# Kernel optimization log

Measured on AMD Instinct MI355X. Metric: run time of the kernel, lower is better.

Reference implementation:

```python
import jax, jax.numpy as jnp
import numpy as np

LN_EPS = 1e-5

def setup_inputs() -> dict:
    key = jax.random.key(0)
    ks = jax.random.split(key, 8)
    B, L, D = 1, 768, 1024
    DP, H, NB = 128, 128, 64
    s = lambda fan_in: 1.0 / np.sqrt(fan_in)
    return {
        "x": jax.random.normal(ks[0], (B, L, D), dtype=jnp.float32),
        "W_down": jax.random.normal(ks[1], (DP, D), dtype=jnp.float32) * s(D),
        "b_down": jax.random.normal(ks[2], (DP,), dtype=jnp.float32) * s(D),
        "W1": jax.random.normal(ks[3], (H, DP), dtype=jnp.float32) * s(DP),
        "b1": jax.random.normal(ks[4], (H,), dtype=jnp.float32) * s(DP),
        "ln_g": jnp.ones((H,), dtype=jnp.float32),
        "ln_b": jnp.zeros((H,), dtype=jnp.float32),
        "W2": jax.random.normal(ks[5], (NB, H), dtype=jnp.float32) * s(H),
        "b2": jax.random.normal(ks[6], (NB,), dtype=jnp.float32) * s(H),
    }

def reference(x, W_down, b_down, W1, b1, ln_g, ln_b, W2, b2):
    # downproject: [B,L,D] -> [B,L,DP]
    xd = jnp.einsum("bld,pd->blp", x, W_down) + b_down
    q, k = jnp.split(xd, 2, axis=-1)                      # each [B,L,DP/2]
    prod = q[:, None, :, :] * k[:, :, None, :]            # [B,L,L,DP/2]
    diff = q[:, None, :, :] - k[:, :, None, :]            # [B,L,L,DP/2]
    h = jnp.concatenate([prod, diff], axis=-1)            # [B,L,L,DP]
    h = jnp.einsum("bijp,hp->bijh", h, W1) + b1           # [B,L,L,H]
    h = jax.nn.gelu(h, approximate=False)                 # torch GELU is exact erf form
    mu = jnp.mean(h, axis=-1, keepdims=True)
    var = jnp.mean(jnp.square(h - mu), axis=-1, keepdims=True)
    h = (h - mu) * jax.lax.rsqrt(var + LN_EPS) * ln_g + ln_b
    out = jnp.einsum("bijh,nh->bijn", h, W2) + b2         # [B,L,L,NB]
    return out
```

## Files before the change

### kernel.cpp

```cpp
#include <hip/hip_runtime.h>
#include <hip/hip_bf16.h>

#define LL 768
#define DD 1024
#define DP 128
#define HP 64
#define HH 128
#define NB 64

typedef float f32x4 __attribute__((ext_vector_type(4)));
typedef __bf16 bf16x8 __attribute__((ext_vector_type(8)));
typedef __bf16 bf16x4 __attribute__((ext_vector_type(4)));

__device__ __forceinline__ float gelu_exact(float x) {
    const float z = fabsf(x) * 0.70710678118654752f;
    const float t = __builtin_amdgcn_rcpf(__builtin_fmaf(0.3275911f, z, 1.0f));
    float p = __builtin_fmaf(t, 1.061405429f, -1.453152027f);
    p = __builtin_fmaf(t, p, 1.421413741f);
    p = __builtin_fmaf(t, p, -0.284496736f);
    p = __builtin_fmaf(t, p, 0.254829592f);
    p = p * t;
    const float e = __expf(-z * z);
    const float erfz = __builtin_fmaf(-p, e, 1.0f);
    const float phi = 0.5f * (1.0f + copysignf(erfz, x));
    return x * phi;
}

__global__ __launch_bounds__(256) void prep_kernel(
    const float* __restrict__ x, const float* __restrict__ Wd,
    const float* __restrict__ bd, const float* __restrict__ W1,
    const float* __restrict__ b1, const float* __restrict__ W2,
    const float* __restrict__ lng, const float* __restrict__ lnb,
    const float* __restrict__ b2,
    __hip_bfloat16* __restrict__ qb, float* __restrict__ kf,
    float* __restrict__ A2, float* __restrict__ Bv,
    __hip_bfloat16* __restrict__ W2gb, float* __restrict__ c2b)
{
    __shared__ __align__(16) float xs[4 * DD];
    __shared__ __align__(16) float xdl[4 * 128];
    const int bid  = blockIdx.x;
    const int tid  = threadIdx.x;
    const int w    = tid >> 6;
    const int lane = tid & 63;

    if (bid >= 192) {
        const int nb = bid - 192;
        for (int e = tid; e < 8 * HH; e += 256) {
            const int n = nb * 8 + (e >> 7), h = e & 127;
            W2gb[n * HH + h] = __float2bfloat16(W2[n * HH + h] * lng[h]);
        }
        #pragma unroll
        for (int rr = 0; rr < 2; ++rr) {
            const int n = nb * 8 + w * 2 + rr;
            float s = W2[n * HH + lane] * lnb[lane]
                    + W2[n * HH + 64 + lane] * lnb[64 + lane];
            #pragma unroll
            for (int m = 1; m < 64; m <<= 1) s += __shfl_xor(s, m);
            if (lane == 0) c2b[n] = s + b2[n];
        }
        return;
    }

    const int l0 = bid * 4;
    const float4* xg = (const float4*)(x + (size_t)l0 * DD);
    float4* xs4 = (float4*)xs;
    for (int idx = tid; idx < 4 * DD / 4; idx += 256) xs4[idx] = xg[idx];
    __syncthreads();

    const int p = tid & 127;
    const int rg = tid >> 7;
    float acc[2] = {0.f, 0.f};
    #pragma unroll 8
    for (int c = 0; c < DD; c += 4) {
        float4 wv = *(const float4*)(Wd + (size_t)p * DD + c);
        #pragma unroll
        for (int rr = 0; rr < 2; ++rr) {
            float4 xv = *(const float4*)(xs + (rg * 2 + rr) * DD + c);
            acc[rr] += wv.x * xv.x + wv.y * xv.y + wv.z * xv.z + wv.w * xv.w;
        }
    }
    const float bdp = bd[p];
    #pragma unroll
    for (int rr = 0; rr < 2; ++rr) {
        const int row = rg * 2 + rr;
        const float v = acc[rr] + bdp;
        xdl[row * 128 + p] = v;
        if (p < HP) qb[(size_t)(l0 + row) * HP + p] = __float2bfloat16(v);
        else        kf[(size_t)(l0 + row) * HP + (p - HP)] = v;
    }
    __syncthreads();

    const int h = tid & 127;
    const int sel = tid >> 7;
    float a4[4] = {0.f, 0.f, 0.f, 0.f};
    #pragma unroll
    for (int c = 0; c < HP; c += 4) {
        float4 wv = *(const float4*)(W1 + (size_t)h * DP + HP + c);
        #pragma unroll
        for (int r = 0; r < 4; ++r) {
            float4 xv = *(const float4*)(xdl + r * 128 + (sel ? HP : 0) + c);
            a4[r] += wv.x * xv.x + wv.y * xv.y + wv.z * xv.z + wv.w * xv.w;
        }
    }
    if (sel == 0) {
        const float bb = b1[h];
        #pragma unroll
        for (int r = 0; r < 4; ++r)
            A2[(size_t)(l0 + r) * HH + h] = a4[r] + bb;
    } else {
        #pragma unroll
        for (int r = 0; r < 4; ++r)
            Bv[(size_t)(l0 + r) * HH + h] = a4[r];
    }
}

__global__ __launch_bounds__(256, 3) void main_kernel(
    const float* __restrict__ W1, const __hip_bfloat16* __restrict__ W2gb,
    const __hip_bfloat16* __restrict__ qb, const float* __restrict__ kf,
    const float* __restrict__ A2, const float* __restrict__ Bv,
    const float* __restrict__ c2b, float* __restrict__ out)
{
    __shared__ __align__(16) unsigned char smem[49152];
    __bf16* Mi   = (__bf16*)smem;
    __bf16* qt   = (__bf16*)(smem + 16384);
    __bf16* W2gs = (__bf16*)(smem + 32768);
    __bf16* hbuf = (__bf16*)smem;

    const int tid  = threadIdx.x;
    const int lane = tid & 63;
    const int w    = tid >> 6;
    const int lo   = lane & 15;
    const int g4   = lane >> 4;
    const int sw   = (lo & 7) << 3;
    const int i    = blockIdx.y;
    const int j0   = blockIdx.x * 128;

    {
        const int hrow = tid >> 1;
        const int pb = (tid & 1) * 32;
        const int swr = (hrow & 7) << 3;
        const float* w1r = W1 + (size_t)hrow * DP + pb;
        const float* kfr = kf + (size_t)i * HP + pb;
        #pragma unroll
        for (int m = 0; m < 4; ++m) {
            float4 w0 = *(const float4*)(w1r + m * 8);
            float4 w1v = *(const float4*)(w1r + m * 8 + 4);
            float4 k0 = *(const float4*)(kfr + m * 8);
            float4 k1 = *(const float4*)(kfr + m * 8 + 4);
            bf16x8 t;
            t[0] = (__bf16)(w0.x * k0.x); t[1] = (__bf16)(w0.y * k0.y);
            t[2] = (__bf16)(w0.z * k0.z); t[3] = (__bf16)(w0.w * k0.w);
            t[4] = (__bf16)(w1v.x * k1.x); t[5] = (__bf16)(w1v.y * k1.y);
            t[6] = (__bf16)(w1v.z * k1.z); t[7] = (__bf16)(w1v.w * k1.w);
            *(bf16x8*)&Mi[hrow * 64 + ((pb + m * 8) ^ swr)] = t;
        }
    }
    {
        const int jl = tid >> 1;
        const int pb = (tid & 1) * 32;
        const int swr = (jl & 7) << 3;
        const unsigned short* src = (const unsigned short*)qb + (size_t)(j0 + jl) * HP + pb;
        #pragma unroll
        for (int m = 0; m < 4; ++m) {
            uint4 v = *(const uint4*)(src + m * 8);
            *(uint4*)&qt[jl * 64 + ((pb + m * 8) ^ swr)] = v;
        }
    }
    {
        const int n = tid >> 2;
        const int hb0 = (tid & 3) * 32;
        const int swr = (n & 7) << 3;
        const unsigned short* src = (const unsigned short*)W2gb + (size_t)n * HH + hb0;
        #pragma unroll
        for (int m = 0; m < 4; ++m) {
            uint4 v = *(const uint4*)(src + m * 8);
            *(uint4*)&W2gs[n * 128 + ((hb0 + m * 8) ^ swr)] = v;
        }
    }
    __syncthreads();

    f32x4 acc[2][8];
    #pragma unroll
    for (int a = 0; a < 2; ++a)
        #pragma unroll
        for (int b = 0; b < 8; ++b)
            #pragma unroll
            for (int e = 0; e < 4; ++e) acc[a][b][e] = 0.f;

    #pragma unroll
    for (int kk = 0; kk < 2; ++kk) {
        const int colx = (kk * 32 + g4 * 8) ^ sw;
        bf16x8 bq[2];
        #pragma unroll
        for (int jt = 0; jt < 2; ++jt)
            bq[jt] = *(const bf16x8*)&qt[(32 * w + jt * 16 + lo) * 64 + colx];
        #pragma unroll
        for (int ht = 0; ht < 8; ++ht) {
            bf16x8 am = *(const bf16x8*)&Mi[(ht * 16 + lo) * 64 + colx];
            #pragma unroll
            for (int jt = 0; jt < 2; ++jt)
                acc[jt][ht] = __builtin_amdgcn_mfma_f32_16x16x32_bf16(am, bq[jt], acc[jt][ht], 0, 0, 0);
        }
    }

    __syncthreads();

    #pragma unroll
    for (int jt = 0; jt < 2; ++jt) {
        const int jl = 32 * w + jt * 16 + lo;
        const float* a2r = A2 + (size_t)(j0 + jl) * HH;
        const float* bvr = Bv + (size_t)i * HH;
        float s = 0.f, ss = 0.f;
        #pragma unroll
        for (int ht = 0; ht < 8; ++ht) {
            const int h4 = ht * 16 + g4 * 4;
            f32x4 a2v = *(const f32x4*)&a2r[h4];
            f32x4 bvv = *(const f32x4*)&bvr[h4];
            #pragma unroll
            for (int r = 0; r < 4; ++r) {
                float v = acc[jt][ht][r] + a2v[r] - bvv[r];
                float g = gelu_exact(v);
                acc[jt][ht][r] = g;
                s += g;
                ss = __builtin_fmaf(g, g, ss);
            }
        }
        s  += __shfl_xor(s, 16);  s  += __shfl_xor(s, 32);
        ss += __shfl_xor(ss, 16); ss += __shfl_xor(ss, 32);
        const float mu   = s * (1.0f / 128.0f);
        const float var  = ss * (1.0f / 128.0f) - mu * mu;
        const float rstd = rsqrtf(var + 1e-5f);
        const float nmr  = -mu * rstd;
        #pragma unroll
        for (int ht = 0; ht < 8; ++ht) {
            bf16x4 t;
            #pragma unroll
            for (int r = 0; r < 4; ++r)
                t[r] = (__bf16)__builtin_fmaf(acc[jt][ht][r], rstd, nmr);
            *(bf16x4*)&hbuf[jl * 128 + ((ht * 16 + g4 * 4) ^ sw)] = t;
        }
    }
    asm volatile("s_waitcnt lgkmcnt(0)" ::: "memory");
    __builtin_amdgcn_sched_barrier(0);

    f32x4 acc2[2][4];
    #pragma unroll
    for (int a = 0; a < 2; ++a)
        #pragma unroll
        for (int b = 0; b < 4; ++b)
            #pragma unroll
            for (int e = 0; e < 4; ++e) acc2[a][b][e] = 0.f;

    #pragma unroll
    for (int kk = 0; kk < 4; ++kk) {
        const int colx = (kk * 32 + g4 * 8) ^ sw;
        bf16x8 bh[2];
        #pragma unroll
        for (int jt = 0; jt < 2; ++jt)
            bh[jt] = *(const bf16x8*)&hbuf[(32 * w + jt * 16 + lo) * 128 + colx];
        #pragma unroll
        for (int nt2 = 0; nt2 < 4; ++nt2) {
            bf16x8 aw = *(const bf16x8*)&W2gs[(nt2 * 16 + lo) * 128 + colx];
            #pragma unroll
            for (int jt = 0; jt < 2; ++jt)
                acc2[jt][nt2] = __builtin_amdgcn_mfma_f32_16x16x32_bf16(aw, bh[jt], acc2[jt][nt2], 0, 0, 0);
        }
    }

    #pragma unroll
    for (int jt = 0; jt < 2; ++jt) {
        const int j = j0 + 32 * w + jt * 16 + lo;
        const size_t base = ((size_t)i * LL + j) * NB;
        #pragma unroll
        for (int nt2 = 0; nt2 < 4; ++nt2) {
            const int n4 = nt2 * 16 + g4 * 4;
            f32x4 c2bv = *(const f32x4*)&c2b[n4];
            f32x4 o;
            #pragma unroll
            for (int r = 0; r < 4; ++r)
                o[r] = acc2[jt][nt2][r] + c2bv[r];
            *(f32x4*)&out[base + n4] = o;
        }
    }
}

extern "C" void kernel_launch(void* const* d_in, const int* in_sizes, int n_in,
                              void* d_out, int out_size, void* d_ws, size_t ws_size,
                              hipStream_t stream) {
    const float* x   = (const float*)d_in[0];
    const float* Wd  = (const float*)d_in[1];
    const float* bd  = (const float*)d_in[2];
    const float* W1  = (const float*)d_in[3];
    const float* b1  = (const float*)d_in[4];
    const float* lng = (const float*)d_in[5];
    const float* lnb = (const float*)d_in[6];
    const float* W2  = (const float*)d_in[7];
    const float* b2  = (const float*)d_in[8];
    float* out = (float*)d_out;

    char* ws = (char*)d_ws;
    __hip_bfloat16* qb   = (__hip_bfloat16*)ws;
    float* kf    = (float*)(ws + 98304);
    float* A2    = (float*)(ws + 294912);
    float* Bv    = (float*)(ws + 688128);
    __hip_bfloat16* W2gb = (__hip_bfloat16*)(ws + 1081344);
    float* c2b   = (float*)(ws + 1097728);

    prep_kernel<<<200, 256, 0, stream>>>(x, Wd, bd, W1, b1, W2, lng, lnb, b2,
                                         qb, kf, A2, Bv, W2gb, c2b);
    dim3 grid(6, 768);
    main_kernel<<<grid, 256, 0, stream>>>(W1, W2gb, qb, kf, A2, Bv, c2b, out);
}
```

Measured before the change: 135.6 us.

## Alias W2 tile into q region and split second GEMM per half-tile

Shared memory drops from 48KB to 32KB. The W2 tile now reuses the q-tile region once the first GEMM finishes, and the H buffer shrinks to 16 rows per wave. The LayerNorm and second GEMM now run one 16-row half at a time, which also cuts the live acc2 registers in half. The W2 global loads are issued into registers before the first GEMM's results are consumed, so their latency overlaps compute. The cost is an extra barrier and less MFMA reuse of each loaded W2 fragment in the second GEMM.

Result: slower. 155.0 us (+14.3%).

```diff
diff --git a/kernel.cpp b/kernel.cpp
--- a/kernel.cpp
+++ b/kernel.cpp
@@ -120,11 +120,11 @@
     const float* __restrict__ A2, const float* __restrict__ Bv,
     const float* __restrict__ c2b, float* __restrict__ out)
 {
-    __shared__ __align__(16) unsigned char smem[49152];
+    __shared__ __align__(16) unsigned char smem[32768];
     __bf16* Mi   = (__bf16*)smem;
     __bf16* qt   = (__bf16*)(smem + 16384);
-    __bf16* W2gs = (__bf16*)(smem + 32768);
     __bf16* hbuf = (__bf16*)smem;
+    __bf16* W2gs = (__bf16*)(smem + 16384);
 
     const int tid  = threadIdx.x;
     const int lane = tid & 63;
@@ -166,50 +166,57 @@
             *(uint4*)&qt[jl * 64 + ((pb + m * 8) ^ swr)] = v;
         }
     }
+    __syncthreads();
+
+    f32x4 acc[2][8];
+    #pragma unroll
+    for (int a = 0; a < 2; ++a)
+        #pragma unroll
+        for (int b = 0; b < 8; ++b)
+            #pragma unroll
+            for (int e = 0; e < 4; ++e) acc[a][b][e] = 0.f;
+
+    #pragma unroll
+    for (int kk = 0; kk < 2; ++kk) {
+        const int colx = (kk * 32 + g4 * 8) ^ sw;
+        bf16x8 bq[2];
+        #pragma unroll
+        for (int jt = 0; jt < 2; ++jt)
+            bq[jt] = *(const bf16x8*)&qt[(32 * w + jt * 16 + lo) * 64 + colx];
+        #pragma unroll
+        for (int ht = 0; ht < 8; ++ht) {
+            bf16x8 am = *(const bf16x8*)&Mi[(ht * 16 + lo) * 64 + colx];
+            #pragma unroll
+            for (int jt = 0; jt < 2; ++jt)
+                acc[jt][ht] = __builtin_amdgcn_mfma_f32_16x16x32_bf16(am, bq[jt], acc[jt][ht], 0, 0, 0);
+        }
+    }
+
+    uint4 wreg[4];
+    {
+        const int n = tid >> 2;
+        const int hb0 = (tid & 3) * 32;
+        const unsigned short* src = (const unsigned short*)W2gb + (size_t)n * HH + hb0;
+        #pragma unroll
+        for (int m = 0; m < 4; ++m)
+            wreg[m] = *(const uint4*)(src + m * 8);
+    }
+    __syncthreads();
     {
         const int n = tid >> 2;
         const int hb0 = (tid & 3) * 32;
         const int swr = (n & 7) << 3;
-        const unsigned short* src = (const unsigned short*)W2gb + (size_t)n * HH + hb0;
-        #pragma unroll
-        for (int m = 0; m < 4; ++m) {
-            uint4 v = *(const uint4*)(src + m * 8);
-            *(uint4*)&W2gs[n * 128 + ((hb0 + m * 8) ^ swr)] = v;
-        }
-    }
-    __syncthreads();
-
-    f32x4 acc[2][8];
-    #pragma unroll
-    for (int a = 0; a < 2; ++a)
-        #pragma unroll
-        for (int b = 0; b < 8; ++b)
-            #pragma unroll
-            for (int e = 0; e < 4; ++e) acc[a][b][e] = 0.f;
-
-    #pragma unroll
-    for (int kk = 0; kk < 2; ++kk) {
-        const int colx = (kk * 32 + g4 * 8) ^ sw;
-        bf16x8 bq[2];
-        #pragma unroll
-        for (int jt = 0; jt < 2; ++jt)
-            bq[jt] = *(const bf16x8*)&qt[(32 * w + jt * 16 + lo) * 64 + colx];
-        #pragma unroll
-        for (int ht = 0; ht < 8; ++ht) {
-            bf16x8 am = *(const bf16x8*)&Mi[(ht * 16 + lo) * 64 + colx];
-            #pragma unroll
-            for (int jt = 0; jt < 2; ++jt)
-                acc[jt][ht] = __builtin_amdgcn_mfma_f32_16x16x32_bf16(am, bq[jt], acc[jt][ht], 0, 0, 0);
-        }
-    }
-
-    __syncthreads();
+        #pragma unroll
+        for (int m = 0; m < 4; ++m)
+            *(uint4*)&W2gs[n * 128 + ((hb0 + m * 8) ^ swr)] = wreg[m];
+    }
+
+    const float* a2base = A2 + (size_t)(j0 + 32 * w + lo) * HH;
+    const float* bvr    = Bv + (size_t)i * HH;
 
     #pragma unroll
     for (int jt = 0; jt < 2; ++jt) {
-        const int jl = 32 * w + jt * 16 + lo;
-        const float* a2r = A2 + (size_t)(j0 + jl) * HH;
-        const float* bvr = Bv + (size_t)i * HH;
+        const float* a2r = a2base + (size_t)(jt * 16) * HH;
         float s = 0.f, ss = 0.f;
         #pragma unroll
         for (int ht = 0; ht < 8; ++ht) {
@@ -231,44 +238,40 @@
         const float var  = ss * (1.0f / 128.0f) - mu * mu;
         const float rstd = rsqrtf(var + 1e-5f);
         const float nmr  = -mu * rstd;
+        const int hrow = w * 16 + lo;
         #pragma unroll
         for (int ht = 0; ht < 8; ++ht) {
             bf16x4 t;
             #pragma unroll
             for (int r = 0; r < 4; ++r)
                 t[r] = (__bf16)__builtin_fmaf(acc[jt][ht][r], rstd, nmr);
-            *(bf16x4*)&hbuf[jl * 128 + ((ht * 16 + g4 * 4) ^ sw)] = t;
-        }
-    }
-    asm volatile("s_waitcnt lgkmcnt(0)" ::: "memory");
-    __builtin_amdgcn_sched_barrier(0);
-
-    f32x4 acc2[2][4];
-    #pragma unroll
-    for (int a = 0; a < 2; ++a)
+            *(bf16x4*)&hbuf[hrow * 128 + ((ht * 16 + g4 * 4) ^ sw)] = t;
+        }
+
+        if (jt == 0) {
+            __syncthreads();
+        } else {
+            asm volatile("s_waitcnt lgkmcnt(0)" ::: "memory");
+            __builtin_amdgcn_sched_barrier(0);
+        }
+
+        f32x4 acc2[4];
         #pragma unroll
         for (int b = 0; b < 4; ++b)
             #pragma unroll
-            for (int e = 0; e < 4; ++e) acc2[a][b][e] = 0.f;
-
-    #pragma unroll
-    for (int kk = 0; kk < 4; ++kk) {
-        const int colx = (kk * 32 + g4 * 8) ^ sw;
-        bf16x8 bh[2];
-        #pragma unroll
-        for (int jt = 0; jt < 2; ++jt)
-            bh[jt] = *(const bf16x8*)&hbuf[(32 * w + jt * 16 + lo) * 128 + colx];
-        #pragma unroll
-        for (int nt2 = 0; nt2 < 4; ++nt2) {
-            bf16x8 aw = *(const bf16x8*)&W2gs[(nt2 * 16 + lo) * 128 + colx];
-            #pragma unroll
-            for (int jt = 0; jt < 2; ++jt)
-                acc2[jt][nt2] = __builtin_amdgcn_mfma_f32_16x16x32_bf16(aw, bh[jt], acc2[jt][nt2], 0, 0, 0);
-        }
-    }
-
-    #pragma unroll
-    for (int jt = 0; jt < 2; ++jt) {
+            for (int e = 0; e < 4; ++e) acc2[b][e] = 0.f;
+
+        #pragma unroll
+        for (int kk = 0; kk < 4; ++kk) {
+            const int colx = (kk * 32 + g4 * 8) ^ sw;
+            bf16x8 bh = *(const bf16x8*)&hbuf[(w * 16 + lo) * 128 + colx];
+            #pragma unroll
+            for (int nt2 = 0; nt2 < 4; ++nt2) {
+                bf16x8 aw = *(const bf16x8*)&W2gs[(nt2 * 16 + lo) * 128 + colx];
+                acc2[nt2] = __builtin_amdgcn_mfma_f32_16x16x32_bf16(aw, bh, acc2[nt2], 0, 0, 0);
+            }
+        }
+
         const int j = j0 + 32 * w + jt * 16 + lo;
         const size_t base = ((size_t)i * LL + j) * NB;
         #pragma unroll
@@ -278,8 +281,13 @@
             f32x4 o;
             #pragma unroll
             for (int r = 0; r < 4; ++r)
-                o[r] = acc2[jt][nt2][r] + c2bv[r];
+                o[r] = acc2[nt2][r] + c2bv[r];
             *(f32x4*)&out[base + n4] = o;
+        }
+
+        if (jt == 0) {
+            asm volatile("s_waitcnt lgkmcnt(0)" ::: "memory");
+            __builtin_amdgcn_sched_barrier(0);
         }
     }
 }
```
